# Optimization experiments

Measured on AMD Instinct MI355X. Metric: run time of the kernel, lower is better.

The kernel has to match this reference:

```python
import jax, jax.numpy as jnp
import numpy as np

# dims
B, T, D, H, A = 256, 64, 6400, 1000, 4
# config['snn'] / config['adaptive_threshold'] values
BETA = 0.9          # 1 - voltage_decay(0.1)
THRESH = 1.0        # threshold_voltage
REST = 0.0          # resting_voltage
THETA_PLUS = 0.05
THETA_DECAY = 0.9


def setup_inputs() -> dict:
    key = jax.random.key(0)
    ks = jax.random.split(key, 7)
    x = jax.random.normal(ks[0], (B, T, D), jnp.float32)
    W1 = jax.random.normal(ks[1], (H, D), jnp.float32) * (1.0 / np.sqrt(D))
    b1 = jax.random.normal(ks[2], (H,), jnp.float32) * 0.01
    W2 = jax.random.normal(ks[3], (A, H), jnp.float32) * (1.0 / np.sqrt(H))
    b2 = jax.random.normal(ks[4], (A,), jnp.float32) * 0.01
    # pre-drawn uniforms for bernoulli sampling at each timestep/layer
    u1 = jax.random.uniform(ks[5], (T, B, H), jnp.float32)
    u2 = jax.random.uniform(ks[6], (T, B, A), jnp.float32)
    return {"x": x, "W1": W1, "b1": b1, "W2": W2, "b2": b2, "u1": u1, "u2": u2}


def _lif(cur, mem, theta, u):
    # StochasticAdaptiveLIF.forward
    mem = BETA * (mem - REST) + REST + cur
    prob = jax.nn.sigmoid(mem - (THRESH + theta))
    spk = (u < prob).astype(mem.dtype)  # bernoulli(prob)
    mem = mem * (1.0 - spk)
    theta = THETA_DECAY * theta + THETA_PLUS * spk
    return spk, mem, theta


def reference(x, W1, b1, W2, b2, u1, u2):
    xT = jnp.swapaxes(x, 0, 1)  # [T, B, D]

    def step(carry, inp):
        mem1, theta1, mem2, theta2 = carry
        xt, u1t, u2t = inp
        cur1 = xt @ W1.T + b1                      # [B, H]
        spk1, mem1, theta1 = _lif(cur1, mem1, theta1, u1t)
        cur2 = spk1 @ W2.T + b2                    # [B, A]
        spk2, mem2, theta2 = _lif(cur2, mem2, theta2, u2t)
        return (mem1, theta1, mem2, theta2), spk2

    init = (jnp.zeros((B, H), x.dtype), jnp.zeros((B, H), x.dtype),
            jnp.zeros((B, A), x.dtype), jnp.zeros((B, A), x.dtype))
    _, spks = jax.lax.scan(step, init, (xT, u1, u2))  # spks: [T, B, A]
    return spks.sum(0) / T
```

## Files before the change

kernel.cpp:

```cpp
#include <hip/hip_runtime.h>
#include <math.h>

#define B_  256
#define T_  64
#define D_  6400
#define H_  1000
#define A_  4

#define BM 128
#define BN 128
#define BK 16

__global__ __launch_bounds__(256) void gemm1_kernel(
    const float* __restrict__ x, const float* __restrict__ W1,
    const float* __restrict__ b1, float* __restrict__ C1) {
  __shared__ float As[BK][BM + 4];
  __shared__ float Bs[BK][BN + 4];

  const int tid = threadIdx.x;
  const int m0 = blockIdx.y * BM;
  const int n0 = blockIdx.x * BN;
  const int tx = tid & 15;
  const int ty = tid >> 4;

  const int row = tid >> 2;
  const int col4 = tid & 3;

  float acc[8][8];
#pragma unroll
  for (int i = 0; i < 8; ++i)
#pragma unroll
    for (int j = 0; j < 8; ++j) acc[i][j] = 0.0f;

  for (int k0 = 0; k0 < D_; k0 += BK) {
    float4 av[2], bv[2];
#pragma unroll
    for (int i = 0; i < 2; ++i) {
      const int r = row + 64 * i;
      av[i] = *(const float4*)(x + (size_t)(m0 + r) * D_ + k0 + col4 * 4);
      const int h = n0 + r;
      if (h < H_) {
        bv[i] = *(const float4*)(W1 + (size_t)h * D_ + k0 + col4 * 4);
      } else {
        bv[i] = make_float4(0.f, 0.f, 0.f, 0.f);
      }
    }
    __syncthreads();
#pragma unroll
    for (int i = 0; i < 2; ++i) {
      const int r = row + 64 * i;
      As[col4 * 4 + 0][r] = av[i].x;
      As[col4 * 4 + 1][r] = av[i].y;
      As[col4 * 4 + 2][r] = av[i].z;
      As[col4 * 4 + 3][r] = av[i].w;
      Bs[col4 * 4 + 0][r] = bv[i].x;
      Bs[col4 * 4 + 1][r] = bv[i].y;
      Bs[col4 * 4 + 2][r] = bv[i].z;
      Bs[col4 * 4 + 3][r] = bv[i].w;
    }
    __syncthreads();
#pragma unroll
    for (int k = 0; k < BK; ++k) {
      const float4 a0 = *(const float4*)&As[k][ty * 8];
      const float4 a1 = *(const float4*)&As[k][ty * 8 + 4];
      const float4 b0 = *(const float4*)&Bs[k][tx * 8];
      const float4 b1v = *(const float4*)&Bs[k][tx * 8 + 4];
      const float ar[8] = {a0.x, a0.y, a0.z, a0.w, a1.x, a1.y, a1.z, a1.w};
      const float br[8] = {b0.x, b0.y, b0.z, b0.w, b1v.x, b1v.y, b1v.z, b1v.w};
#pragma unroll
      for (int i = 0; i < 8; ++i)
#pragma unroll
        for (int j = 0; j < 8; ++j) acc[i][j] = fmaf(ar[i], br[j], acc[i][j]);
    }
    __syncthreads();
  }

  const int h0 = n0 + tx * 8;
  if (h0 < H_) {
    float bias[8];
#pragma unroll
    for (int j = 0; j < 8; ++j) bias[j] = b1[h0 + j];
#pragma unroll
    for (int i = 0; i < 8; ++i) {
      const int m = m0 + ty * 8 + i;
      const int bb = m >> 6;
      const int tt = m & 63;
      float* op = C1 + (size_t)tt * (B_ * H_) + (size_t)bb * H_ + h0;
      float4 r0, r1;
      r0.x = acc[i][0] + bias[0];
      r0.y = acc[i][1] + bias[1];
      r0.z = acc[i][2] + bias[2];
      r0.w = acc[i][3] + bias[3];
      r1.x = acc[i][4] + bias[4];
      r1.y = acc[i][5] + bias[5];
      r1.z = acc[i][6] + bias[6];
      r1.w = acc[i][7] + bias[7];
      *(float4*)(op) = r0;
      *(float4*)(op + 4) = r1;
    }
  }
}

__device__ __forceinline__ float sigmoid_f(float z) {
  return 1.0f / (1.0f + expf(-z));
}

__global__ __launch_bounds__(256) void snn_seq_kernel(
    const float* __restrict__ C1, const float* __restrict__ u1,
    const float* __restrict__ W2, const float* __restrict__ b2,
    const float* __restrict__ u2, float* __restrict__ out) {
  const int b = blockIdx.x;
  const int tid = threadIdx.x;
  const int lane = tid & 63;
  const int wv = tid >> 6;

  __shared__ float sW2[A_ * H_];
  __shared__ float sRed[4][A_];

  for (int i = tid; i < A_ * H_; i += 256) sW2[i] = W2[i];
  __syncthreads();

  float mem1[4] = {0.f, 0.f, 0.f, 0.f};
  float th1[4] = {0.f, 0.f, 0.f, 0.f};
  float mem2[A_] = {0.f, 0.f, 0.f, 0.f};
  float th2[A_] = {0.f, 0.f, 0.f, 0.f};
  float scnt[A_] = {0.f, 0.f, 0.f, 0.f};

  for (int t = 0; t < T_; ++t) {
    const float* c1p = C1 + (size_t)t * (B_ * H_) + (size_t)b * H_;
    const float* u1p = u1 + (size_t)t * (B_ * H_) + (size_t)b * H_;
    float part[A_] = {0.f, 0.f, 0.f, 0.f};
#pragma unroll
    for (int k = 0; k < 4; ++k) {
      const int h = k * 256 + tid;
      if (h < H_) {
        const float cur = c1p[h];
        float m = fmaf(0.9f, mem1[k], cur);
        const float z = m - (1.0f + th1[k]);
        const float p = sigmoid_f(z);
        const float spk = (u1p[h] < p) ? 1.0f : 0.0f;
        m = (spk != 0.0f) ? 0.0f : m;
        th1[k] = fmaf(0.9f, th1[k], 0.05f * spk);
        mem1[k] = m;
        if (spk != 0.0f) {
          part[0] += sW2[h];
          part[1] += sW2[H_ + h];
          part[2] += sW2[2 * H_ + h];
          part[3] += sW2[3 * H_ + h];
        }
      }
    }
#pragma unroll
    for (int off = 32; off >= 1; off >>= 1) {
#pragma unroll
      for (int a = 0; a < A_; ++a) part[a] += __shfl_down(part[a], off);
    }
    if (lane == 0) {
      sRed[wv][0] = part[0];
      sRed[wv][1] = part[1];
      sRed[wv][2] = part[2];
      sRed[wv][3] = part[3];
    }
    __syncthreads();
    if (tid == 0) {
#pragma unroll
      for (int a = 0; a < A_; ++a) {
        const float cur2 =
            sRed[0][a] + sRed[1][a] + sRed[2][a] + sRed[3][a] + b2[a];
        float m = fmaf(0.9f, mem2[a], cur2);
        const float z = m - (1.0f + th2[a]);
        const float p = sigmoid_f(z);
        const float u = u2[(size_t)t * (B_ * A_) + b * A_ + a];
        const float spk = (u < p) ? 1.0f : 0.0f;
        mem2[a] = (spk != 0.0f) ? 0.0f : m;
        th2[a] = fmaf(0.9f, th2[a], 0.05f * spk);
        scnt[a] += spk;
      }
    }
    __syncthreads();
  }

  if (tid == 0) {
#pragma unroll
    for (int a = 0; a < A_; ++a) out[b * A_ + a] = scnt[a] * (1.0f / 64.0f);
  }
}

extern "C" void kernel_launch(void* const* d_in, const int* in_sizes, int n_in,
                              void* d_out, int out_size, void* d_ws,
                              size_t ws_size, hipStream_t stream) {
  const float* x = (const float*)d_in[0];
  const float* W1 = (const float*)d_in[1];
  const float* b1 = (const float*)d_in[2];
  const float* W2 = (const float*)d_in[3];
  const float* b2 = (const float*)d_in[4];
  const float* u1 = (const float*)d_in[5];
  const float* u2 = (const float*)d_in[6];
  float* out = (float*)d_out;
  float* C1 = (float*)d_ws;

  dim3 g1((H_ + BN - 1) / BN, (B_ * T_) / BM);
  gemm1_kernel<<<g1, 256, 0, stream>>>(x, W1, b1, C1);
  snn_seq_kernel<<<B_, 256, 0, stream>>>(C1, u1, W2, b2, u2, out);
}
```

Measured before the change: 3.414 ms.

## Prefetch next GEMM tile into registers and interleave per-thread LDS fragments

The fp32 GEMM main loop now issues global loads for the next K-slice before computing on the current shared-memory tile. Global latency can then overlap the FMA work, and the trailing barrier is dropped. Each thread's 8x8 output block is split into two 4-wide halves 64 apart in both M and N, which reduces LDS bank conflicts on the float4 fragment reads. The epilogue is updated to match the new mapping and guards each half against H overflow. The cost is extra live registers for the prefetched tile, which could lower occupancy.

```diff
diff --git a/kernel.cpp b/kernel.cpp
--- a/kernel.cpp
+++ b/kernel.cpp
@@ -32,19 +32,17 @@
 #pragma unroll
     for (int j = 0; j < 8; ++j) acc[i][j] = 0.0f;
 
+  float4 av[2], bv[2];
+#pragma unroll
+  for (int i = 0; i < 2; ++i) {
+    const int r = row + 64 * i;
+    av[i] = *(const float4*)(x + (size_t)(m0 + r) * D_ + col4 * 4);
+    const int h = n0 + r;
+    bv[i] = (h < H_) ? *(const float4*)(W1 + (size_t)h * D_ + col4 * 4)
+                     : make_float4(0.f, 0.f, 0.f, 0.f);
+  }
+
   for (int k0 = 0; k0 < D_; k0 += BK) {
-    float4 av[2], bv[2];
-#pragma unroll
-    for (int i = 0; i < 2; ++i) {
-      const int r = row + 64 * i;
-      av[i] = *(const float4*)(x + (size_t)(m0 + r) * D_ + k0 + col4 * 4);
-      const int h = n0 + r;
-      if (h < H_) {
-        bv[i] = *(const float4*)(W1 + (size_t)h * D_ + k0 + col4 * 4);
-      } else {
-        bv[i] = make_float4(0.f, 0.f, 0.f, 0.f);
-      }
-    }
     __syncthreads();
 #pragma unroll
     for (int i = 0; i < 2; ++i) {
@@ -59,12 +57,23 @@
       Bs[col4 * 4 + 3][r] = bv[i].w;
     }
     __syncthreads();
+    if (k0 + BK < D_) {
+      const int kn = k0 + BK;
+#pragma unroll
+      for (int i = 0; i < 2; ++i) {
+        const int r = row + 64 * i;
+        av[i] = *(const float4*)(x + (size_t)(m0 + r) * D_ + kn + col4 * 4);
+        const int h = n0 + r;
+        bv[i] = (h < H_) ? *(const float4*)(W1 + (size_t)h * D_ + kn + col4 * 4)
+                         : make_float4(0.f, 0.f, 0.f, 0.f);
+      }
+    }
 #pragma unroll
     for (int k = 0; k < BK; ++k) {
-      const float4 a0 = *(const float4*)&As[k][ty * 8];
-      const float4 a1 = *(const float4*)&As[k][ty * 8 + 4];
-      const float4 b0 = *(const float4*)&Bs[k][tx * 8];
-      const float4 b1v = *(const float4*)&Bs[k][tx * 8 + 4];
+      const float4 a0 = *(const float4*)&As[k][ty * 4];
+      const float4 a1 = *(const float4*)&As[k][64 + ty * 4];
+      const float4 b0 = *(const float4*)&Bs[k][tx * 4];
+      const float4 b1v = *(const float4*)&Bs[k][64 + tx * 4];
       const float ar[8] = {a0.x, a0.y, a0.z, a0.w, a1.x, a1.y, a1.z, a1.w};
       const float br[8] = {b0.x, b0.y, b0.z, b0.w, b1v.x, b1v.y, b1v.z, b1v.w};
 #pragma unroll
@@ -72,31 +81,39 @@
 #pragma unroll
         for (int j = 0; j < 8; ++j) acc[i][j] = fmaf(ar[i], br[j], acc[i][j]);
     }
-    __syncthreads();
-  }
-
-  const int h0 = n0 + tx * 8;
-  if (h0 < H_) {
-    float bias[8];
-#pragma unroll
-    for (int j = 0; j < 8; ++j) bias[j] = b1[h0 + j];
-#pragma unroll
-    for (int i = 0; i < 8; ++i) {
-      const int m = m0 + ty * 8 + i;
+  }
+
+  const int h0 = n0 + tx * 4;
+  const int h1 = n0 + 64 + tx * 4;
+  float4 bias0 = (h0 < H_) ? *(const float4*)(b1 + h0)
+                           : make_float4(0.f, 0.f, 0.f, 0.f);
+  float4 bias1 = (h1 < H_) ? *(const float4*)(b1 + h1)
+                           : make_float4(0.f, 0.f, 0.f, 0.f);
+#pragma unroll
+  for (int ih = 0; ih < 2; ++ih) {
+#pragma unroll
+    for (int i2 = 0; i2 < 4; ++i2) {
+      const int i = ih * 4 + i2;
+      const int m = m0 + ih * 64 + ty * 4 + i2;
       const int bb = m >> 6;
       const int tt = m & 63;
-      float* op = C1 + (size_t)tt * (B_ * H_) + (size_t)bb * H_ + h0;
-      float4 r0, r1;
-      r0.x = acc[i][0] + bias[0];
-      r0.y = acc[i][1] + bias[1];
-      r0.z = acc[i][2] + bias[2];
-      r0.w = acc[i][3] + bias[3];
-      r1.x = acc[i][4] + bias[4];
-      r1.y = acc[i][5] + bias[5];
-      r1.z = acc[i][6] + bias[6];
-      r1.w = acc[i][7] + bias[7];
-      *(float4*)(op) = r0;
-      *(float4*)(op + 4) = r1;
+      float* op = C1 + (size_t)tt * (B_ * H_) + (size_t)bb * H_;
+      if (h0 < H_) {
+        float4 r0;
+        r0.x = acc[i][0] + bias0.x;
+        r0.y = acc[i][1] + bias0.y;
+        r0.z = acc[i][2] + bias0.z;
+        r0.w = acc[i][3] + bias0.w;
+        *(float4*)(op + h0) = r0;
+      }
+      if (h1 < H_) {
+        float4 r1;
+        r1.x = acc[i][4] + bias1.x;
+        r1.y = acc[i][5] + bias1.y;
+        r1.z = acc[i][6] + bias1.z;
+        r1.w = acc[i][7] + bias1.w;
+        *(float4*)(op + h1) = r1;
+      }
     }
   }
 }
```

Result: faster. 3.216 ms (-5.8%).
